# Optimization experiments

Hardware: AMD Instinct MI355X
Metric: run time of the kernel (lower is better)

Reference implementation:

```python
import jax, jax.numpy as jnp
import numpy as np

D = 2            # stalk dimension d
FD = 3           # final_d = d + 1 (add_lp=True, add_hp=False)
HID = 32         # hidden_channels
N_NODES = 50000
E0 = 200000      # undirected edges; directed edge list has 2*E0 entries (second half reversed)
IN_CH = 128
OUT_CH = 32
N_LAYERS = 2
PSIZE = D * (D + 1) // 2  # cayley param size per edge


def _spectral_normalize(W, iters=20):
    # torch spectral_norm: power iteration with detached u, v; sigma = u^T W v
    u = jnp.full((W.shape[0],), 1.0 / np.sqrt(W.shape[0]), W.dtype)
    def body(_, u):
        v = W.T @ u
        v = v / (jnp.linalg.norm(v) + 1e-12)
        u2 = W @ v
        return u2 / (jnp.linalg.norm(u2) + 1e-12)
    u = jax.lax.fori_loop(0, iters, body, u)
    u = jax.lax.stop_gradient(u)
    v = jax.lax.stop_gradient(W.T @ u)
    v = v / (jnp.linalg.norm(v) + 1e-12)
    return W / (u @ W @ v)


def _cayley(p):
    # p: [E, PSIZE] lower-tri params -> skew A -> orthogonal Q = (I - A)^{-1}(I + A)
    E = p.shape[0]
    r, c = jnp.tril_indices(D)
    M = jnp.zeros((E, D, D), p.dtype).at[:, r, c].set(p)
    A = M - jnp.swapaxes(M, 1, 2)
    I = jnp.eye(D, dtype=p.dtype)
    return jnp.linalg.solve(I[None] - A, I[None] + A)


def setup_inputs() -> dict:
    key = jax.random.key(0)
    ks = jax.random.split(key, 8)
    src = jax.random.randint(ks[0], (E0,), 0, N_NODES)
    dst = jax.random.randint(ks[1], (E0,), 0, N_NODES)
    # symmetric directed edge list; edge j and edge j+E0 are reverses of each other
    edge_index = jnp.concatenate([jnp.stack([src, dst]), jnp.stack([dst, src])], axis=1)
    x = jax.random.normal(ks[2], (N_NODES, IN_CH), jnp.float32)
    s = 0.02
    W1 = jax.random.normal(ks[3], (FD * HID, IN_CH), jnp.float32) * s
    b1 = jnp.zeros((FD * HID,), jnp.float32)
    W2 = jax.random.normal(ks[4], (OUT_CH, FD * HID), jnp.float32) * s
    b2 = jnp.zeros((OUT_CH,), jnp.float32)
    W_left = jnp.tile(jnp.eye(FD, dtype=jnp.float32)[None], (N_LAYERS, 1, 1))  # init eye per torch
    W_right = jax.random.normal(ks[5], (N_LAYERS, HID, HID), jnp.float32) / np.sqrt(HID)
    eps = jnp.zeros((N_LAYERS, FD, 1), jnp.float32)
    W_sheaf = jax.random.normal(ks[6], (N_LAYERS, PSIZE, 2 * FD * HID), jnp.float32) * s
    W_wt = jax.random.normal(ks[7], (N_LAYERS, 1, 2 * FD * HID), jnp.float32) * s
    return {"x": x, "edge_index": edge_index, "W1": W1, "b1": b1, "W2": W2, "b2": b2,
            "W_left": W_left, "W_right": W_right, "eps": eps, "W_sheaf": W_sheaf, "W_wt": W_wt}


def reference(x, edge_index, W1, b1, W2, b2, W_left, W_right, eps, W_sheaf, W_wt):
    N = x.shape[0]
    row, col = edge_index[0], edge_index[1]
    e0 = row.shape[0] // 2
    rev = jnp.concatenate([jnp.arange(e0) + e0, jnp.arange(e0)])  # reverse-edge index
    # lin1 + ELU (dropouts = 0 in eval)
    h = jax.nn.elu(x @ W1.T + b1)                 # [N, FD*HID]
    xc = h.reshape(N * FD, HID)                   # [N*FD, HID]
    x0 = xc
    for layer in range(N_LAYERS):
        # --- sheaf learner + edge weight learner (gather endpoint features) ---
        xn = xc.reshape(N, FD * HID)
        cat = jnp.concatenate([xn[row], xn[col]], axis=-1)   # [2*E0, 2*FD*HID]
        p = jnp.tanh(cat @ W_sheaf[layer].T)                 # sheaf map params [2*E0, PSIZE]
        wdir = jax.nn.sigmoid(cat @ W_wt[layer].T)[:, 0]
        w = wdir * wdir[rev]                                 # symmetric edge weight
        # --- normalized connection (bundle) Laplacian ---
        Q = _cayley(p)                                       # per-edge orthogonal maps
        T = jnp.einsum('eij,eik->ejk', Q, Q[rev])            # transport F_u^T F_v
        w2 = w * w
        deg = jax.ops.segment_sum(w2, row, num_segments=N)
        dinv = jnp.where(deg > 0, jax.lax.rsqrt(jnp.maximum(deg, 1e-30)), 0.0)
        cnorm = w2 * dinv[row] * dinv[col]                   # [2*E0]
        # --- left / right weights (spectral-normalized) ---
        Wl = _spectral_normalize(W_left[layer])
        Wr = _spectral_normalize(W_right[layer])
        y = xc.reshape(N, FD, HID)
        y = jnp.einsum('ef,nfh->neh', Wl, y)                 # mix stalk dims
        y = jnp.einsum('neh,ch->nec', y, Wr)                 # mix channels
        # --- apply block-sparse Laplacian: Lx[u] = x[u] - sum_e c_e B_e x[v] ---
        yv = y[col]                                          # gather  [2*E0, FD, HID]
        tv = jnp.concatenate([jnp.einsum('eij,ejh->eih', T, yv[:, :D]), yv[:, D:]], axis=1)
        agg = jax.ops.segment_sum(cnorm[:, None, None] * tv, row, num_segments=N)
        diag = jnp.where(deg > 0, 1.0, 0.0)[:, None, None]
        z = jax.nn.elu((diag * y - agg).reshape(N * FD, HID))
        # --- epsilon-gated residual ---
        coeff = jnp.tile(1.0 + jnp.tanh(eps[layer]), (N, 1))  # [N*FD, 1]
        x0 = coeff * x0 - z
        xc = x0
    return xc.reshape(N, FD * HID) @ W2.T + b2
```

## Files before the change

kernel.cpp:

```cpp
#include <hip/hip_runtime.h>

#define NN 50000
#define E0 200000
#define E2 400000
#define NGROUPS ((NN + 7) / 8)
#define NCHUNK  ((NN + 255) / 256)
#define NTILES  ((NN + 63) / 64)
#define EB      ((E2 + 255) / 256)

typedef __attribute__((ext_vector_type(8))) short short8;
typedef __attribute__((ext_vector_type(4))) float f32x4;

__device__ __forceinline__ float eluf(float x) { return x > 0.0f ? x : expm1f(x); }
__device__ __forceinline__ float fsig(float x) { return 1.0f / (1.0f + __expf(-x)); }
__device__ __forceinline__ float ftanh(float x) {
    float e = __expf(-2.0f * x);
    return (1.0f - e) / (1.0f + e);
}
__device__ __forceinline__ unsigned rne_bf16(float x) {
    unsigned u = __float_as_uint(x);
    return (u + 0x7fffu + ((u >> 16) & 1u)) >> 16;
}

__global__ __launch_bounds__(256) void k_setup(const float* __restrict__ Wl_in, const float* __restrict__ Wr_in,
                                               float* __restrict__ Wl_out, float* __restrict__ Wr_out,
                                               int* __restrict__ cnt, int* __restrict__ fill,
                                               float* __restrict__ deg0, int* __restrict__ gtotal) {
    __shared__ float W[32 * 33];
    __shared__ float us[32], vs[32], tmp[32];
    __shared__ float scal;
    int t = threadIdx.x;
    if (blockIdx.x < 2) {
        int l = blockIdx.x;
        for (int i = t; i < 1024; i += 256) W[(i >> 5) * 33 + (i & 31)] = Wr_in[l * 1024 + i];
        if (t < 32) us[t] = 0.17677669529663688f;
        __syncthreads();
        for (int it = 0; it < 20; ++it) {
            if (t < 32) { float a = 0; for (int r = 0; r < 32; ++r) a = fmaf(W[r * 33 + t], us[r], a); tmp[t] = a; }
            __syncthreads();
            if (t == 0) { float s = 0; for (int c = 0; c < 32; ++c) s += tmp[c] * tmp[c]; scal = 1.0f / (sqrtf(s) + 1e-12f); }
            __syncthreads();
            if (t < 32) vs[t] = tmp[t] * scal;
            __syncthreads();
            if (t < 32) { float a = 0; for (int c = 0; c < 32; ++c) a = fmaf(W[t * 33 + c], vs[c], a); tmp[t] = a; }
            __syncthreads();
            if (t == 0) { float s = 0; for (int r = 0; r < 32; ++r) s += tmp[r] * tmp[r]; scal = 1.0f / (sqrtf(s) + 1e-12f); }
            __syncthreads();
            if (t < 32) us[t] = tmp[t] * scal;
            __syncthreads();
        }
        if (t < 32) { float a = 0; for (int r = 0; r < 32; ++r) a = fmaf(W[r * 33 + t], us[r], a); tmp[t] = a; }
        __syncthreads();
        if (t == 0) {
            float s = 0; for (int c = 0; c < 32; ++c) s += tmp[c] * tmp[c];
            scal = (sqrtf(s) + 1e-12f) / s;
        }
        __syncthreads();
        for (int i = t; i < 1024; i += 256) Wr_out[l * 1024 + i] = W[(i >> 5) * 33 + (i & 31)] * scal;
        if (t == 0) {
            float M[9];
            for (int i = 0; i < 9; ++i) M[i] = Wl_in[l * 9 + i];
            float u[3] = {0.5773502691896258f, 0.5773502691896258f, 0.5773502691896258f};
            float v[3], u2[3];
            for (int it = 0; it < 20; ++it) {
                float s = 0;
                for (int c = 0; c < 3; ++c) { v[c] = M[c] * u[0] + M[3 + c] * u[1] + M[6 + c] * u[2]; s += v[c] * v[c]; }
                float inv = 1.0f / (sqrtf(s) + 1e-12f);
                for (int c = 0; c < 3; ++c) v[c] *= inv;
                s = 0;
                for (int r = 0; r < 3; ++r) { u2[r] = M[r * 3] * v[0] + M[r * 3 + 1] * v[1] + M[r * 3 + 2] * v[2]; s += u2[r] * u2[r]; }
                inv = 1.0f / (sqrtf(s) + 1e-12f);
                for (int r = 0; r < 3; ++r) u[r] = u2[r] * inv;
            }
            float s = 0;
            for (int c = 0; c < 3; ++c) { v[c] = M[c] * u[0] + M[3 + c] * u[1] + M[6 + c] * u[2]; s += v[c] * v[c]; }
            float inv = (sqrtf(s) + 1e-12f) / s;
            for (int i = 0; i < 9; ++i) Wl_out[l * 9 + i] = M[i] * inv;
        }
    } else {
        int base = (blockIdx.x - 2) * 256 + t;
        int stride = (gridDim.x - 2) * 256;
        if (blockIdx.x == 2 && t == 0) *gtotal = 0;
        for (int i = base; i < NN; i += stride) { cnt[i] = 0; fill[i] = 0; deg0[i] = 0.0f; }
    }
}

template<int K, int N, int NH, bool ELU, bool HIST>
__global__ __launch_bounds__(256) void k_gemm(const float* __restrict__ X,
                                              const float* __restrict__ W,
                                              const float* __restrict__ bias,
                                              float* __restrict__ out,
                                              const int* __restrict__ row, int* __restrict__ cnt) {
    constexpr int KP = K + 8;
    constexpr int NT = NH / 16;
    constexpr int KS = K / 32;
    constexpr int NHALVES = N / NH;
    __shared__ __align__(16) unsigned short whi[NH * KP];
    __shared__ __align__(16) unsigned short wlo[NH * KP];
    int tid = threadIdx.x;
    if (HIST) {
        for (int e = blockIdx.x * 256 + tid; e < E2; e += gridDim.x * 256)
            atomicAdd(&cnt[row[e]], 1);
    }
    const int ch = blockIdx.x % NHALVES;
    const int tstream = blockIdx.x / NHALVES;
    const int nstreams = gridDim.x / NHALVES;
    for (int i = tid; i < NH * K; i += 256) {
        float v = W[ch * NH * K + i];
        int r = i / K, c = i % K;
        unsigned h = rne_bf16(v);
        whi[r * KP + c] = (unsigned short)h;
        wlo[r * KP + c] = (unsigned short)rne_bf16(v - __uint_as_float(h << 16));
    }
    __syncthreads();
    int wave = tid >> 6, lane = tid & 63;
    int quad = lane >> 4, r16 = lane & 15;
    for (int t = tstream; t < NTILES; t += nstreams) {
        long m = (long)t * 64 + wave * 16 + r16;
        long mc = m < NN ? m : (NN - 1);
        const float* xrow = X + mc * K + quad * 8;
        short8 ah[KS], al[KS];
#pragma unroll
        for (int ks = 0; ks < KS; ++ks) {
            const float4* xp = (const float4*)(xrow + ks * 32);
            float4 p0 = xp[0], p1 = xp[1];
            float xv[8] = {p0.x, p0.y, p0.z, p0.w, p1.x, p1.y, p1.z, p1.w};
#pragma unroll
            for (int j = 0; j < 8; ++j) {
                unsigned h = rne_bf16(xv[j]);
                ah[ks][j] = (short)h;
                al[ks][j] = (short)rne_bf16(xv[j] - __uint_as_float(h << 16));
            }
        }
        long mbase = (long)t * 64 + wave * 16 + quad * 4;
#pragma unroll
        for (int tt = 0; tt < NT; ++tt) {
            f32x4 acc = (f32x4){0.f, 0.f, 0.f, 0.f};
#pragma unroll
            for (int ks = 0; ks < KS; ++ks) {
                int ro = (tt * 16 + r16) * KP + ks * 32 + quad * 8;
                short8 bh = *(const short8*)&whi[ro];
                short8 bl = *(const short8*)&wlo[ro];
                acc = __builtin_amdgcn_mfma_f32_16x16x32_bf16(ah[ks], bh, acc, 0, 0, 0);
                acc = __builtin_amdgcn_mfma_f32_16x16x32_bf16(al[ks], bh, acc, 0, 0, 0);
                acc = __builtin_amdgcn_mfma_f32_16x16x32_bf16(ah[ks], bl, acc, 0, 0, 0);
            }
            int coln = ch * NH + tt * 16 + r16;
            float b = bias[coln];
#pragma unroll
            for (int rr = 0; rr < 4; ++rr) {
                long mm = mbase + rr;
                if (mm < NN) {
                    float v = acc[rr] + b;
                    if (ELU) v = eluf(v);
                    out[mm * N + coln] = v;
                }
            }
        }
    }
}

__global__ __launch_bounds__(256) void k_scan(const int* __restrict__ cnt, int* __restrict__ start,
                                              int* __restrict__ gtotal) {
    __shared__ int s[256];
    __shared__ int soff;
    int b = blockIdx.x, t = threadIdx.x;
    int i = b * 256 + t;
    int v = (i < NN) ? cnt[i] : 0;
    s[t] = v;
    __syncthreads();
    for (int off = 1; off < 256; off <<= 1) {
        int add = (t >= off) ? s[t - off] : 0;
        __syncthreads();
        s[t] += add;
        __syncthreads();
    }
    if (t == 255) soff = atomicAdd(gtotal, s[255]);
    __syncthreads();
    if (i < NN) start[i] = s[t] - v + soff;
}

__global__ __launch_bounds__(256) void k_filly8(const float* __restrict__ xc,
                                                const float* __restrict__ Wl, const float* __restrict__ Wr,
                                                const float* __restrict__ Wsh, const float* __restrict__ Wwt,
                                                unsigned* __restrict__ yA, unsigned short* __restrict__ yB,
                                                float4* __restrict__ proj,
                                                const int* __restrict__ row, const int* __restrict__ start,
                                                int* __restrict__ fill, int* __restrict__ eslot) {
    int tid = threadIdx.x;
    if (blockIdx.x >= NGROUPS) {
        int e = (blockIdx.x - NGROUPS) * 256 + tid;
        if (e < E2) {
            int u = row[e];
            eslot[e] = start[u] + atomicAdd(&fill[u], 1);
        }
        return;
    }
    __shared__ float wrs[32 * 33];
    __shared__ float wls[9];
    __shared__ float xcs[8][96];
    __shared__ float ws1[192], wt[192];
    int n0 = blockIdx.x * 8;
    for (int i = tid; i < 1024; i += 256) wrs[(i >> 5) * 33 + (i & 31)] = Wr[i];
    if (tid < 9) wls[tid] = Wl[tid];
    if (tid < 192) {
        ws1[tid] = Wsh[192 + tid];
        wt[tid]  = Wwt[tid];
    }
    for (int i = tid; i < 192; i += 256) {
        int nd = i / 24, of = (i % 24) * 4;
        *(float4*)&xcs[nd][of] = *(const float4*)&xc[(n0 + nd) * 96 + of];
    }
    __syncthreads();
    int node = tid >> 5, c = tid & 31;
    int n = n0 + node;
    float a1 = 0, a2 = 0, a3 = 0, a4 = 0;
#pragma unroll
    for (int j = 0; j < 3; ++j) {
        int k = j * 32 + c;
        float xv = xcs[node][k];
        a1 = fmaf(xv, ws1[k], a1);
        a2 = fmaf(xv, ws1[96 + k], a2);
        a3 = fmaf(xv, wt[k], a3);
        a4 = fmaf(xv, wt[96 + k], a4);
    }
#pragma unroll
    for (int off = 16; off; off >>= 1) {
        a1 += __shfl_xor(a1, off);
        a2 += __shfl_xor(a2, off);
        a3 += __shfl_xor(a3, off);
        a4 += __shfl_xor(a4, off);
    }
    if (c == 0) proj[n] = make_float4(a1, a2, a3, a4);
    {
        float t0 = 0, t1 = 0, t2 = 0;
        const float* wr = &wrs[c * 33];
        const float* xr = xcs[node];
#pragma unroll
        for (int h = 0; h < 32; ++h) {
            float w = wr[h];
            t0 = fmaf(xr[h], w, t0);
            t1 = fmaf(xr[32 + h], w, t1);
            t2 = fmaf(xr[64 + h], w, t2);
        }
        float o0 = wls[0] * t0 + wls[1] * t1 + wls[2] * t2;
        float o1 = wls[3] * t0 + wls[4] * t1 + wls[5] * t2;
        float o2 = wls[6] * t0 + wls[7] * t1 + wls[8] * t2;
        yA[n * 32 + c] = rne_bf16(o0) | (rne_bf16(o1) << 16);
        yB[n * 32 + c] = (unsigned short)rne_bf16(o2);
    }
}

__global__ __launch_bounds__(256) void k_coef(const int* __restrict__ row, const int* __restrict__ col,
                                              const int* __restrict__ eslot,
                                              const float4* __restrict__ proj,
                                              uint2* __restrict__ meta, float* __restrict__ deg) {
    int e = blockIdx.x * 256 + threadIdx.x;
    if (e >= E0) return;
    int u = row[e], v = col[e];
    float4 pu = proj[u], pv = proj[v];
    float a_e = ftanh(pu.x + pv.y);
    float a_r = ftanh(pv.x + pu.y);
    float wd_e = fsig(pu.z + pv.w);
    float wd_r = fsig(pv.z + pu.w);
    float w = wd_e * wd_r;
    float w2 = w * w;
    float ie = 1.0f / (1.0f + a_e * a_e), ir = 1.0f / (1.0f + a_r * a_r);
    float ce = (1.0f - a_e * a_e) * ie, se = 2.0f * a_e * ie;
    float cr = (1.0f - a_r * a_r) * ir, sr = 2.0f * a_r * ir;
    float C = ce * cr + se * sr;
    float S = ce * sr - se * cr;
    unsigned cb = rne_bf16(C), sb = rne_bf16(S), wb = rne_bf16(w2);
    meta[eslot[e]]      = make_uint2(cb | (sb << 16), (unsigned)v | (wb << 16));
    meta[eslot[e + E0]] = make_uint2(cb | ((sb ^ 0x8000u) << 16), (unsigned)u | (wb << 16));
    atomicAdd(&deg[u], w2);
    atomicAdd(&deg[v], w2);
}

__device__ __forceinline__ void gather_accum(int s0, int ec, int c,
                                             const uint2* __restrict__ meta,
                                             const float* __restrict__ deg, float du,
                                             const unsigned* __restrict__ yA,
                                             const unsigned short* __restrict__ yB,
                                             float& acc0, float& acc1, float& acc2) {
    for (int bs = 0; bs < ec; bs += 32) {
        int nb2 = min(32, ec - bs);
        float CC = 0, SS = 0, cnl = 0;
        int vj = 0;
        if (c < nb2) {
            uint2 mt = meta[s0 + bs + c];
            vj = (int)(mt.y & 0xffffu);
            float w2 = __uint_as_float(mt.y & 0xffff0000u);
            float Cv = __uint_as_float(mt.x << 16);
            float Sv = __uint_as_float(mt.x & 0xffff0000u);
            float dv = deg[vj];
            float dvi = dv > 0.0f ? rsqrtf(fmaxf(dv, 1e-30f)) : 0.0f;
            cnl = w2 * du * dvi;
            CC = cnl * Cv;
            SS = cnl * Sv;
        }
        int j4 = nb2 & ~3;
        int j = 0;
        for (; j < j4; j += 4) {
#pragma unroll
            for (int jj = 0; jj < 4; ++jj) {
                float Cj = __shfl(CC, j + jj, 32);
                float Sj = __shfl(SS, j + jj, 32);
                float cj = __shfl(cnl, j + jj, 32);
                int v = __shfl(vj, j + jj, 32);
                unsigned ua = yA[v * 32 + c];
                unsigned ub = (unsigned)yB[v * 32 + c];
                float y0 = __uint_as_float(ua << 16);
                float y1 = __uint_as_float(ua & 0xffff0000u);
                float y2 = __uint_as_float(ub << 16);
                acc0 = fmaf(Cj, y0, acc0);
                acc0 = fmaf(-Sj, y1, acc0);
                acc1 = fmaf(Sj, y0, acc1);
                acc1 = fmaf(Cj, y1, acc1);
                acc2 = fmaf(cj, y2, acc2);
            }
        }
        for (; j < nb2; ++j) {
            float Cj = __shfl(CC, j, 32);
            float Sj = __shfl(SS, j, 32);
            float cj = __shfl(cnl, j, 32);
            int v = __shfl(vj, j, 32);
            unsigned ua = yA[v * 32 + c];
            unsigned ub = (unsigned)yB[v * 32 + c];
            float y0 = __uint_as_float(ua << 16);
            float y1 = __uint_as_float(ua & 0xffff0000u);
            float y2 = __uint_as_float(ub << 16);
            acc0 = fmaf(Cj, y0, acc0);
            acc0 = fmaf(-Sj, y1, acc0);
            acc1 = fmaf(Sj, y0, acc1);
            acc1 = fmaf(Cj, y1, acc1);
            acc2 = fmaf(cj, y2, acc2);
        }
    }
}

__global__ __launch_bounds__(256) void k_gatherY(const int* __restrict__ start,
                                                 const int* __restrict__ cnt,
                                                 const uint2* __restrict__ meta,
                                                 const float* __restrict__ deg0,
                                                 const unsigned* __restrict__ yA0,
                                                 const unsigned short* __restrict__ yB0,
                                                 const float* __restrict__ eps,
                                                 float* __restrict__ xc,
                                                 const float* __restrict__ Wl, const float* __restrict__ Wr,
                                                 const float* __restrict__ Wsh, const float* __restrict__ Wwt,
                                                 unsigned* __restrict__ yA1, unsigned short* __restrict__ yB1,
                                                 float4* __restrict__ proj, float* __restrict__ deg1) {
    __shared__ float wrs[32 * 33];
    __shared__ float wls[9];
    __shared__ float xcs[8][96];
    __shared__ float ws1[192], wt[192];
    int tid = threadIdx.x;
    for (int i = tid; i < 1024; i += 256) wrs[(i >> 5) * 33 + (i & 31)] = Wr[i];
    if (tid < 9) wls[tid] = Wl[tid];
    if (tid < 192) {
        ws1[tid] = Wsh[(1 * 3 + 1) * 192 + tid];
        wt[tid]  = Wwt[1 * 192 + tid];
    }
    int node = tid >> 5, c = tid & 31;
    int n = blockIdx.x * 8 + node;
    int s0 = start[n], ec = cnt[n];
    float dn = deg0[n];
    float du = dn > 0.0f ? rsqrtf(fmaxf(dn, 1e-30f)) : 0.0f;
    float acc0 = 0, acc1 = 0, acc2 = 0;
    gather_accum(s0, ec, c, meta, deg0, du, yA0, yB0, acc0, acc1, acc2);
    float diag = dn > 0.0f ? 1.0f : 0.0f;
    unsigned ua = yA0[n * 32 + c];
    unsigned ub = (unsigned)yB0[n * 32 + c];
    float oy0 = __uint_as_float(ua << 16);
    float oy1 = __uint_as_float(ua & 0xffff0000u);
    float oy2 = __uint_as_float(ub << 16);
    float c0 = 1.0f + tanhf(eps[0]);
    float c1 = 1.0f + tanhf(eps[1]);
    float c2 = 1.0f + tanhf(eps[2]);
    int base = n * 96 + c;
    float nx0 = c0 * xc[base]      - eluf(diag * oy0 - acc0);
    float nx1 = c1 * xc[base + 32] - eluf(diag * oy1 - acc1);
    float nx2 = c2 * xc[base + 64] - eluf(diag * oy2 - acc2);
    xc[base] = nx0; xc[base + 32] = nx1; xc[base + 64] = nx2;
    if (c == 0) deg1[n] = 0.0f;
    xcs[node][c] = nx0; xcs[node][32 + c] = nx1; xcs[node][64 + c] = nx2;
    __syncthreads();
    float a1 = nx0 * ws1[c] + nx1 * ws1[32 + c] + nx2 * ws1[64 + c];
    float a2 = nx0 * ws1[96 + c] + nx1 * ws1[128 + c] + nx2 * ws1[160 + c];
    float a3 = nx0 * wt[c] + nx1 * wt[32 + c] + nx2 * wt[64 + c];
    float a4 = nx0 * wt[96 + c] + nx1 * wt[128 + c] + nx2 * wt[160 + c];
#pragma unroll
    for (int off = 16; off; off >>= 1) {
        a1 += __shfl_xor(a1, off);
        a2 += __shfl_xor(a2, off);
        a3 += __shfl_xor(a3, off);
        a4 += __shfl_xor(a4, off);
    }
    if (c == 0) proj[n] = make_float4(a1, a2, a3, a4);
    {
        float t0 = 0, t1 = 0, t2 = 0;
        const float* wr = &wrs[c * 33];
        const float* xr = xcs[node];
#pragma unroll
        for (int h = 0; h < 32; ++h) {
            float w = wr[h];
            t0 = fmaf(xr[h], w, t0);
            t1 = fmaf(xr[32 + h], w, t1);
            t2 = fmaf(xr[64 + h], w, t2);
        }
        float o0 = wls[0] * t0 + wls[1] * t1 + wls[2] * t2;
        float o1 = wls[3] * t0 + wls[4] * t1 + wls[5] * t2;
        float o2 = wls[6] * t0 + wls[7] * t1 + wls[8] * t2;
        yA1[n * 32 + c] = rne_bf16(o0) | (rne_bf16(o1) << 16);
        yB1[n * 32 + c] = (unsigned short)rne_bf16(o2);
    }
}

__global__ __launch_bounds__(256) void k_gather(const int* __restrict__ start,
                                                const int* __restrict__ cnt,
                                                const uint2* __restrict__ meta,
                                                const float* __restrict__ deg,
                                                const unsigned* __restrict__ yA,
                                                const unsigned short* __restrict__ yB,
                                                const float* __restrict__ eps,
                                                int layer, float* __restrict__ xc) {
    int tid = threadIdx.x;
    int node = tid >> 5, c = tid & 31;
    int n = blockIdx.x * 8 + node;
    if (n >= NN) return;
    int s0 = start[n], ec = cnt[n];
    float dn = deg[n];
    float du = dn > 0.0f ? rsqrtf(fmaxf(dn, 1e-30f)) : 0.0f;
    float acc0 = 0, acc1 = 0, acc2 = 0;
    gather_accum(s0, ec, c, meta, deg, du, yA, yB, acc0, acc1, acc2);
    float diag = dn > 0.0f ? 1.0f : 0.0f;
    unsigned ua = yA[n * 32 + c];
    unsigned ub = (unsigned)yB[n * 32 + c];
    float oy0 = __uint_as_float(ua << 16);
    float oy1 = __uint_as_float(ua & 0xffff0000u);
    float oy2 = __uint_as_float(ub << 16);
    float c0 = 1.0f + tanhf(eps[layer * 3 + 0]);
    float c1 = 1.0f + tanhf(eps[layer * 3 + 1]);
    float c2 = 1.0f + tanhf(eps[layer * 3 + 2]);
    int base = n * 96 + c;
    float z0 = eluf(diag * oy0 - acc0);
    float z1 = eluf(diag * oy1 - acc1);
    float z2 = eluf(diag * oy2 - acc2);
    xc[base]      = c0 * xc[base]      - z0;
    xc[base + 32] = c1 * xc[base + 32] - z1;
    xc[base + 64] = c2 * xc[base + 64] - z2;
}

extern "C" void kernel_launch(void* const* d_in, const int* in_sizes, int n_in,
                              void* d_out, int out_size, void* d_ws, size_t ws_size,
                              hipStream_t stream) {
    const float* x     = (const float*)d_in[0];
    const int*   ei    = (const int*)d_in[1];
    const float* W1    = (const float*)d_in[2];
    const float* b1    = (const float*)d_in[3];
    const float* W2    = (const float*)d_in[4];
    const float* b2    = (const float*)d_in[5];
    const float* Wl    = (const float*)d_in[6];
    const float* Wr    = (const float*)d_in[7];
    const float* eps   = (const float*)d_in[8];
    const float* Wsh   = (const float*)d_in[9];
    const float* Wwt   = (const float*)d_in[10];
    float* out = (float*)d_out;
    const int* row = ei;
    const int* col = ei + E2;

    char* pc = (char*)d_ws;
    float* xc     = (float*)pc;          pc += (size_t)NN * 96 * 4;
    uint2* meta   = (uint2*)pc;          pc += (size_t)E2 * 8;
    unsigned* yA0 = (unsigned*)pc;       pc += (size_t)NN * 32 * 4;
    unsigned* yA1 = (unsigned*)pc;       pc += (size_t)NN * 32 * 4;
    unsigned short* yB0 = (unsigned short*)pc; pc += (size_t)NN * 32 * 2;
    unsigned short* yB1 = (unsigned short*)pc; pc += (size_t)NN * 32 * 2;
    pc = (char*)(((size_t)pc + 15) & ~(size_t)15);
    float4* proj  = (float4*)pc;         pc += (size_t)NN * 16;
    float* deg0   = (float*)pc;          pc += (size_t)NN * 4;
    float* deg1   = (float*)pc;          pc += (size_t)NN * 4;
    float* Wl_n   = (float*)pc;          pc += 32 * 4;
    float* Wr_n   = (float*)pc;          pc += 2048 * 4;
    int* cnt      = (int*)pc;            pc += (size_t)NN * 4;
    int* start    = (int*)pc;            pc += (size_t)NN * 4;
    int* fill     = (int*)pc;            pc += (size_t)NN * 4;
    int* eslot    = (int*)pc;            pc += (size_t)E2 * 4;
    int* gtotal   = (int*)pc;            pc += 4;

    k_setup<<<34, 256, 0, stream>>>(Wl, Wr, Wl_n, Wr_n, cnt, fill, deg0, gtotal);
    k_gemm<128, 96, 48, true, true><<<512, 256, 0, stream>>>(x, W1, b1, xc, row, cnt);
    k_scan<<<NCHUNK, 256, 0, stream>>>(cnt, start, gtotal);
    k_filly8<<<NGROUPS + EB, 256, 0, stream>>>(xc, Wl_n, Wr_n, Wsh, Wwt,
                                               yA0, yB0, proj, row, start, fill, eslot);
    k_coef<<<(E0 + 255) / 256, 256, 0, stream>>>(row, col, eslot, proj, meta, deg0);
    k_gatherY<<<NGROUPS, 256, 0, stream>>>(start, cnt, meta, deg0, yA0, yB0, eps, xc,
                                           Wl_n + 9, Wr_n + 1024, Wsh, Wwt, yA1, yB1, proj, deg1);
    k_coef<<<(E0 + 255) / 256, 256, 0, stream>>>(row, col, eslot, proj, meta, deg1);
    k_gather<<<NGROUPS, 256, 0, stream>>>(start, cnt, meta, deg1, yA1, yB1, eps, 1, xc);
    k_gemm<96, 32, 32, false, false><<<512, 256, 0, stream>>>(xc, W2, b2, out, nullptr, nullptr);
}
```

Measured before the change: 321.7 us.

## Split gather across two half-waves per node, pack y into uint2, move spectral norm into gemm

```diff
diff --git a/kernel.cpp b/kernel.cpp
--- a/kernel.cpp
+++ b/kernel.cpp
@@ -4,6 +4,7 @@
 #define E0 200000
 #define E2 400000
 #define NGROUPS ((NN + 7) / 8)
+#define NG4     ((NN + 3) / 4)
 #define NCHUNK  ((NN + 255) / 256)
 #define NTILES  ((NN + 63) / 64)
 #define EB      ((E2 + 255) / 256)
@@ -22,89 +23,96 @@
     return (u + 0x7fffu + ((u >> 16) & 1u)) >> 16;
 }
 
-__global__ __launch_bounds__(256) void k_setup(const float* __restrict__ Wl_in, const float* __restrict__ Wr_in,
-                                               float* __restrict__ Wl_out, float* __restrict__ Wr_out,
-                                               int* __restrict__ cnt, int* __restrict__ fill,
+__global__ __launch_bounds__(256) void k_setup(int* __restrict__ cnt, int* __restrict__ fill,
                                                float* __restrict__ deg0, int* __restrict__ gtotal) {
+    int i = blockIdx.x * 256 + threadIdx.x;
+    if (i == 0) *gtotal = 0;
+    if (i < NN) { cnt[i] = 0; fill[i] = 0; deg0[i] = 0.0f; }
+}
+
+__device__ __forceinline__ void spectral_block(int l, const float* __restrict__ Wl_in,
+                                               const float* __restrict__ Wr_in,
+                                               float* __restrict__ Wl_out, float* __restrict__ Wr_out) {
     __shared__ float W[32 * 33];
     __shared__ float us[32], vs[32], tmp[32];
     __shared__ float scal;
     int t = threadIdx.x;
-    if (blockIdx.x < 2) {
-        int l = blockIdx.x;
-        for (int i = t; i < 1024; i += 256) W[(i >> 5) * 33 + (i & 31)] = Wr_in[l * 1024 + i];
-        if (t < 32) us[t] = 0.17677669529663688f;
-        __syncthreads();
+    for (int i = t; i < 1024; i += 256) W[(i >> 5) * 33 + (i & 31)] = Wr_in[l * 1024 + i];
+    if (t < 32) us[t] = 0.17677669529663688f;
+    __syncthreads();
+    for (int it = 0; it < 20; ++it) {
+        if (t < 32) { float a = 0; for (int r = 0; r < 32; ++r) a = fmaf(W[r * 33 + t], us[r], a); tmp[t] = a; }
+        __syncthreads();
+        if (t == 0) { float s = 0; for (int c = 0; c < 32; ++c) s += tmp[c] * tmp[c]; scal = 1.0f / (sqrtf(s) + 1e-12f); }
+        __syncthreads();
+        if (t < 32) vs[t] = tmp[t] * scal;
+        __syncthreads();
+        if (t < 32) { float a = 0; for (int c = 0; c < 32; ++c) a = fmaf(W[t * 33 + c], vs[c], a); tmp[t] = a; }
+        __syncthreads();
+        if (t == 0) { float s = 0; for (int r = 0; r < 32; ++r) s += tmp[r] * tmp[r]; scal = 1.0f / (sqrtf(s) + 1e-12f); }
+        __syncthreads();
+        if (t < 32) us[t] = tmp[t] * scal;
+        __syncthreads();
+    }
+    if (t < 32) { float a = 0; for (int r = 0; r < 32; ++r) a = fmaf(W[r * 33 + t], us[r], a); tmp[t] = a; }
+    __syncthreads();
+    if (t == 0) {
+        float s = 0; for (int c = 0; c < 32; ++c) s += tmp[c] * tmp[c];
+        scal = (sqrtf(s) + 1e-12f) / s;
+    }
+    __syncthreads();
+    for (int i = t; i < 1024; i += 256) Wr_out[l * 1024 + i] = W[(i >> 5) * 33 + (i & 31)] * scal;
+    if (t == 0) {
+        float M[9];
+        for (int i = 0; i < 9; ++i) M[i] = Wl_in[l * 9 + i];
+        float u[3] = {0.5773502691896258f, 0.5773502691896258f, 0.5773502691896258f};
+        float v[3], u2[3];
         for (int it = 0; it < 20; ++it) {
-            if (t < 32) { float a = 0; for (int r = 0; r < 32; ++r) a = fmaf(W[r * 33 + t], us[r], a); tmp[t] = a; }
-            __syncthreads();
-            if (t == 0) { float s = 0; for (int c = 0; c < 32; ++c) s += tmp[c] * tmp[c]; scal = 1.0f / (sqrtf(s) + 1e-12f); }
-            __syncthreads();
-            if (t < 32) vs[t] = tmp[t] * scal;
-            __syncthreads();
-            if (t < 32) { float a = 0; for (int c = 0; c < 32; ++c) a = fmaf(W[t * 33 + c], vs[c], a); tmp[t] = a; }
-            __syncthreads();
-            if (t == 0) { float s = 0; for (int r = 0; r < 32; ++r) s += tmp[r] * tmp[r]; scal = 1.0f / (sqrtf(s) + 1e-12f); }
-            __syncthreads();
-            if (t < 32) us[t] = tmp[t] * scal;
-            __syncthreads();
-        }
-        if (t < 32) { float a = 0; for (int r = 0; r < 32; ++r) a = fmaf(W[r * 33 + t], us[r], a); tmp[t] = a; }
-        __syncthreads();
-        if (t == 0) {
-            float s = 0; for (int c = 0; c < 32; ++c) s += tmp[c] * tmp[c];
-            scal = (sqrtf(s) + 1e-12f) / s;
-        }
-        __syncthreads();
-        for (int i = t; i < 1024; i += 256) Wr_out[l * 1024 + i] = W[(i >> 5) * 33 + (i & 31)] * scal;
-        if (t == 0) {
-            float M[9];
-            for (int i = 0; i < 9; ++i) M[i] = Wl_in[l * 9 + i];
-            float u[3] = {0.5773502691896258f, 0.5773502691896258f, 0.5773502691896258f};
-            float v[3], u2[3];
-            for (int it = 0; it < 20; ++it) {
-                float s = 0;
-                for (int c = 0; c < 3; ++c) { v[c] = M[c] * u[0] + M[3 + c] * u[1] + M[6 + c] * u[2]; s += v[c] * v[c]; }
-                float inv = 1.0f / (sqrtf(s) + 1e-12f);
-                for (int c = 0; c < 3; ++c) v[c] *= inv;
-                s = 0;
-                for (int r = 0; r < 3; ++r) { u2[r] = M[r * 3] * v[0] + M[r * 3 + 1] * v[1] + M[r * 3 + 2] * v[2]; s += u2[r] * u2[r]; }
-                inv = 1.0f / (sqrtf(s) + 1e-12f);
-                for (int r = 0; r < 3; ++r) u[r] = u2[r] * inv;
-            }
             float s = 0;
             for (int c = 0; c < 3; ++c) { v[c] = M[c] * u[0] + M[3 + c] * u[1] + M[6 + c] * u[2]; s += v[c] * v[c]; }
-            float inv = (sqrtf(s) + 1e-12f) / s;
-            for (int i = 0; i < 9; ++i) Wl_out[l * 9 + i] = M[i] * inv;
-        }
-    } else {
-        int base = (blockIdx.x - 2) * 256 + t;
-        int stride = (gridDim.x - 2) * 256;
-        if (blockIdx.x == 2 && t == 0) *gtotal = 0;
-        for (int i = base; i < NN; i += stride) { cnt[i] = 0; fill[i] = 0; deg0[i] = 0.0f; }
-    }
-}
-
-template<int K, int N, int NH, bool ELU, bool HIST>
+            float inv = 1.0f / (sqrtf(s) + 1e-12f);
+            for (int c = 0; c < 3; ++c) v[c] *= inv;
+            s = 0;
+            for (int r = 0; r < 3; ++r) { u2[r] = M[r * 3] * v[0] + M[r * 3 + 1] * v[1] + M[r * 3 + 2] * v[2]; s += u2[r] * u2[r]; }
+            inv = 1.0f / (sqrtf(s) + 1e-12f);
+            for (int r = 0; r < 3; ++r) u[r] = u2[r] * inv;
+        }
+        float s = 0;
+        for (int c = 0; c < 3; ++c) { v[c] = M[c] * u[0] + M[3 + c] * u[1] + M[6 + c] * u[2]; s += v[c] * v[c]; }
+        float inv = (sqrtf(s) + 1e-12f) / s;
+        for (int i = 0; i < 9; ++i) Wl_out[l * 9 + i] = M[i] * inv;
+    }
+}
+
+template<int K, int N, int NH, bool ELU, bool AUX>
 __global__ __launch_bounds__(256) void k_gemm(const float* __restrict__ X,
                                               const float* __restrict__ W,
                                               const float* __restrict__ bias,
                                               float* __restrict__ out,
-                                              const int* __restrict__ row, int* __restrict__ cnt) {
+                                              const int* __restrict__ row, int* __restrict__ cnt,
+                                              const float* __restrict__ Wl_in, const float* __restrict__ Wr_in,
+                                              float* __restrict__ Wl_out, float* __restrict__ Wr_out) {
     constexpr int KP = K + 8;
     constexpr int NT = NH / 16;
     constexpr int KS = K / 32;
     constexpr int NHALVES = N / NH;
+    const int nmain = AUX ? (int)gridDim.x - 2 : (int)gridDim.x;
+    if constexpr (AUX) {
+        if ((int)blockIdx.x >= nmain) {
+            spectral_block((int)blockIdx.x - nmain, Wl_in, Wr_in, Wl_out, Wr_out);
+            return;
+        }
+    }
     __shared__ __align__(16) unsigned short whi[NH * KP];
     __shared__ __align__(16) unsigned short wlo[NH * KP];
     int tid = threadIdx.x;
-    if (HIST) {
-        for (int e = blockIdx.x * 256 + tid; e < E2; e += gridDim.x * 256)
+    if constexpr (AUX) {
+        for (int e = blockIdx.x * 256 + tid; e < E2; e += nmain * 256)
             atomicAdd(&cnt[row[e]], 1);
     }
     const int ch = blockIdx.x % NHALVES;
     const int tstream = blockIdx.x / NHALVES;
-    const int nstreams = gridDim.x / NHALVES;
+    const int nstreams = nmain / NHALVES;
     for (int i = tid; i < NH * K; i += 256) {
         float v = W[ch * NH * K + i];
         int r = i / K, c = i % K;
@@ -183,7 +191,7 @@
 __global__ __launch_bounds__(256) void k_filly8(const float* __restrict__ xc,
                                                 const float* __restrict__ Wl, const float* __restrict__ Wr,
                                                 const float* __restrict__ Wsh, const float* __restrict__ Wwt,
-                                                unsigned* __restrict__ yA, unsigned short* __restrict__ yB,
+                                                uint2* __restrict__ yAB,
                                                 float4* __restrict__ proj,
                                                 const int* __restrict__ row, const int* __restrict__ start,
                                                 int* __restrict__ fill, int* __restrict__ eslot) {
@@ -246,8 +254,7 @@
         float o0 = wls[0] * t0 + wls[1] * t1 + wls[2] * t2;
         float o1 = wls[3] * t0 + wls[4] * t1 + wls[5] * t2;
         float o2 = wls[6] * t0 + wls[7] * t1 + wls[8] * t2;
-        yA[n * 32 + c] = rne_bf16(o0) | (rne_bf16(o1) << 16);
-        yB[n * 32 + c] = (unsigned short)rne_bf16(o2);
+        yAB[n * 32 + c] = make_uint2(rne_bf16(o0) | (rne_bf16(o1) << 16), rne_bf16(o2) << 16);
     }
 }
 
@@ -277,18 +284,19 @@
     atomicAdd(&deg[v], w2);
 }
 
-__device__ __forceinline__ void gather_accum(int s0, int ec, int c,
+__device__ __forceinline__ void gather_accum(int s0, int ec, int h, int c,
                                              const uint2* __restrict__ meta,
                                              const float* __restrict__ deg, float du,
-                                             const unsigned* __restrict__ yA,
-                                             const unsigned short* __restrict__ yB,
+                                             const uint2* __restrict__ yAB,
                                              float& acc0, float& acc1, float& acc2) {
-    for (int bs = 0; bs < ec; bs += 32) {
-        int nb2 = min(32, ec - bs);
+    const uint2* yc = yAB + c;
+    for (int bs = 0; bs < ec; bs += 64) {
+        int nb = min(64, ec - bs);
         float CC = 0, SS = 0, cnl = 0;
         int vj = 0;
-        if (c < nb2) {
-            uint2 mt = meta[s0 + bs + c];
+        int eidx = 2 * c + h;
+        if (eidx < nb) {
+            uint2 mt = meta[s0 + bs + eidx];
             vj = (int)(mt.y & 0xffffu);
             float w2 = __uint_as_float(mt.y & 0xffff0000u);
             float Cv = __uint_as_float(mt.x << 16);
@@ -299,7 +307,8 @@
             CC = cnl * Cv;
             SS = cnl * Sv;
         }
-        int j4 = nb2 & ~3;
+        int jmax = (nb + 1 - h) >> 1;
+        int j4 = jmax & ~3;
         int j = 0;
         for (; j < j4; j += 4) {
 #pragma unroll
@@ -308,11 +317,10 @@
                 float Sj = __shfl(SS, j + jj, 32);
                 float cj = __shfl(cnl, j + jj, 32);
                 int v = __shfl(vj, j + jj, 32);
-                unsigned ua = yA[v * 32 + c];
-                unsigned ub = (unsigned)yB[v * 32 + c];
-                float y0 = __uint_as_float(ua << 16);
-                float y1 = __uint_as_float(ua & 0xffff0000u);
-                float y2 = __uint_as_float(ub << 16);
+                uint2 y = yc[v * 32];
+                float y0 = __uint_as_float(y.x << 16);
+                float y1 = __uint_as_float(y.x & 0xffff0000u);
+                float y2 = __uint_as_float(y.y);
                 acc0 = fmaf(Cj, y0, acc0);
                 acc0 = fmaf(-Sj, y1, acc0);
                 acc1 = fmaf(Sj, y0, acc1);
@@ -320,16 +328,15 @@
                 acc2 = fmaf(cj, y2, acc2);
             }
         }
-        for (; j < nb2; ++j) {
+        for (; j < jmax; ++j) {
             float Cj = __shfl(CC, j, 32);
             float Sj = __shfl(SS, j, 32);
             float cj = __shfl(cnl, j, 32);
             int v = __shfl(vj, j, 32);
-            unsigned ua = yA[v * 32 + c];
-            unsigned ub = (unsigned)yB[v * 32 + c];
-            float y0 = __uint_as_float(ua << 16);
-            float y1 = __uint_as_float(ua & 0xffff0000u);
-            float y2 = __uint_as_float(ub << 16);
+            uint2 y = yc[v * 32];
+            float y0 = __uint_as_float(y.x << 16);
+            float y1 = __uint_as_float(y.x & 0xffff0000u);
+            float y2 = __uint_as_float(y.y);
             acc0 = fmaf(Cj, y0, acc0);
             acc0 = fmaf(-Sj, y1, acc0);
             acc1 = fmaf(Sj, y0, acc1);
@@ -343,49 +350,53 @@
                                                  const int* __restrict__ cnt,
                                                  const uint2* __restrict__ meta,
                                                  const float* __restrict__ deg0,
-                                                 const unsigned* __restrict__ yA0,
-                                                 const unsigned short* __restrict__ yB0,
+                                                 const uint2* __restrict__ yAB0,
                                                  const float* __restrict__ eps,
                                                  float* __restrict__ xc,
                                                  const float* __restrict__ Wl, const float* __restrict__ Wr,
                                                  const float* __restrict__ Wsh, const float* __restrict__ Wwt,
-                                                 unsigned* __restrict__ yA1, unsigned short* __restrict__ yB1,
+                                                 uint2* __restrict__ yAB1,
                                                  float4* __restrict__ proj, float* __restrict__ deg1) {
     __shared__ float wrs[32 * 33];
     __shared__ float wls[9];
-    __shared__ float xcs[8][96];
+    __shared__ float xcs[4][96];
     __shared__ float ws1[192], wt[192];
     int tid = threadIdx.x;
     for (int i = tid; i < 1024; i += 256) wrs[(i >> 5) * 33 + (i & 31)] = Wr[i];
     if (tid < 9) wls[tid] = Wl[tid];
     if (tid < 192) {
         ws1[tid] = Wsh[(1 * 3 + 1) * 192 + tid];
-        wt[tid]  = Wwt[1 * 192 + tid];
-    }
-    int node = tid >> 5, c = tid & 31;
-    int n = blockIdx.x * 8 + node;
+        wt[tid]  = Wwt[192 + tid];
+    }
+    int wv = tid >> 6, lane = tid & 63, h = lane >> 5, c = lane & 31;
+    int n = blockIdx.x * 4 + wv;
     int s0 = start[n], ec = cnt[n];
     float dn = deg0[n];
     float du = dn > 0.0f ? rsqrtf(fmaxf(dn, 1e-30f)) : 0.0f;
-    float acc0 = 0, acc1 = 0, acc2 = 0;
-    gather_accum(s0, ec, c, meta, deg0, du, yA0, yB0, acc0, acc1, acc2);
-    float diag = dn > 0.0f ? 1.0f : 0.0f;
-    unsigned ua = yA0[n * 32 + c];
-    unsigned ub = (unsigned)yB0[n * 32 + c];
-    float oy0 = __uint_as_float(ua << 16);
-    float oy1 = __uint_as_float(ua & 0xffff0000u);
-    float oy2 = __uint_as_float(ub << 16);
+    int base = n * 96 + c;
+    float xv0 = xc[base], xv1 = xc[base + 32], xv2 = xc[base + 64];
+    uint2 yown = yAB0[n * 32 + c];
     float c0 = 1.0f + tanhf(eps[0]);
     float c1 = 1.0f + tanhf(eps[1]);
     float c2 = 1.0f + tanhf(eps[2]);
-    int base = n * 96 + c;
-    float nx0 = c0 * xc[base]      - eluf(diag * oy0 - acc0);
-    float nx1 = c1 * xc[base + 32] - eluf(diag * oy1 - acc1);
-    float nx2 = c2 * xc[base + 64] - eluf(diag * oy2 - acc2);
-    xc[base] = nx0; xc[base + 32] = nx1; xc[base + 64] = nx2;
-    if (c == 0) deg1[n] = 0.0f;
-    xcs[node][c] = nx0; xcs[node][32 + c] = nx1; xcs[node][64 + c] = nx2;
-    __syncthreads();
+    __syncthreads();
+    float acc0 = 0, acc1 = 0, acc2 = 0;
+    gather_accum(s0, ec, h, c, meta, deg0, du, yAB0, acc0, acc1, acc2);
+    acc0 += __shfl_xor(acc0, 32);
+    acc1 += __shfl_xor(acc1, 32);
+    acc2 += __shfl_xor(acc2, 32);
+    float diag = dn > 0.0f ? 1.0f : 0.0f;
+    float oy0 = __uint_as_float(yown.x << 16);
+    float oy1 = __uint_as_float(yown.x & 0xffff0000u);
+    float oy2 = __uint_as_float(yown.y);
+    float nx0 = c0 * xv0 - eluf(diag * oy0 - acc0);
+    float nx1 = c1 * xv1 - eluf(diag * oy1 - acc1);
+    float nx2 = c2 * xv2 - eluf(diag * oy2 - acc2);
+    if (h == 0) {
+        xc[base] = nx0; xc[base + 32] = nx1; xc[base + 64] = nx2;
+        xcs[wv][c] = nx0; xcs[wv][32 + c] = nx1; xcs[wv][64 + c] = nx2;
+        if (c == 0) deg1[n] = 0.0f;
+    }
     float a1 = nx0 * ws1[c] + nx1 * ws1[32 + c] + nx2 * ws1[64 + c];
     float a2 = nx0 * ws1[96 + c] + nx1 * ws1[128 + c] + nx2 * ws1[160 + c];
     float a3 = nx0 * wt[c] + nx1 * wt[32 + c] + nx2 * wt[64 + c];
@@ -397,23 +408,26 @@
         a3 += __shfl_xor(a3, off);
         a4 += __shfl_xor(a4, off);
     }
-    if (c == 0) proj[n] = make_float4(a1, a2, a3, a4);
-    {
-        float t0 = 0, t1 = 0, t2 = 0;
-        const float* wr = &wrs[c * 33];
-        const float* xr = xcs[node];
-#pragma unroll
-        for (int h = 0; h < 32; ++h) {
-            float w = wr[h];
-            t0 = fmaf(xr[h], w, t0);
-            t1 = fmaf(xr[32 + h], w, t1);
-            t2 = fmaf(xr[64 + h], w, t2);
-        }
+    if (lane == 0) proj[n] = make_float4(a1, a2, a3, a4);
+    __syncthreads();
+    float t0 = 0, t1 = 0, t2 = 0;
+    const float* wr = &wrs[c * 33 + h * 16];
+    const float* xr = &xcs[wv][h * 16];
+#pragma unroll
+    for (int k = 0; k < 16; ++k) {
+        float w = wr[k];
+        t0 = fmaf(xr[k], w, t0);
+        t1 = fmaf(xr[32 + k], w, t1);
+        t2 = fmaf(xr[64 + k], w, t2);
+    }
+    t0 += __shfl_xor(t0, 32);
+    t1 += __shfl_xor(t1, 32);
+    t2 += __shfl_xor(t2, 32);
+    if (h == 0) {
         float o0 = wls[0] * t0 + wls[1] * t1 + wls[2] * t2;
         float o1 = wls[3] * t0 + wls[4] * t1 + wls[5] * t2;
         float o2 = wls[6] * t0 + wls[7] * t1 + wls[8] * t2;
-        yA1[n * 32 + c] = rne_bf16(o0) | (rne_bf16(o1) << 16);
-        yB1[n * 32 + c] = (unsigned short)rne_bf16(o2);
+        yAB1[n * 32 + c] = make_uint2(rne_bf16(o0) | (rne_bf16(o1) << 16), rne_bf16(o2) << 16);
     }
 }
 
@@ -421,35 +435,35 @@
                                                 const int* __restrict__ cnt,
                                                 const uint2* __restrict__ meta,
                                                 const float* __restrict__ deg,
-                                                const unsigned* __restrict__ yA,
-                                                const unsigned short* __restrict__ yB,
+                                                const uint2* __restrict__ yAB,
                                                 const float* __restrict__ eps,
                                                 int layer, float* __restrict__ xc) {
     int tid = threadIdx.x;
-    int node = tid >> 5, c = tid & 31;
-    int n = blockIdx.x * 8 + node;
-    if (n >= NN) return;
+    int lane = tid & 63, h = lane >> 5, c = lane & 31;
+    int n = blockIdx.x * 4 + (tid >> 6);
     int s0 = start[n], ec = cnt[n];
     float dn = deg[n];
     float du = dn > 0.0f ? rsqrtf(fmaxf(dn, 1e-30f)) : 0.0f;
-    float acc0 = 0, acc1 = 0, acc2 = 0;
-    gather_accum(s0, ec, c, meta, deg, du, yA, yB, acc0, acc1, acc2);
-    float diag = dn > 0.0f ? 1.0f : 0.0f;
-    unsigned ua = yA[n * 32 + c];
-    unsigned ub = (unsigned)yB[n * 32 + c];
-    float oy0 = __uint_as_float(ua << 16);
-    float oy1 = __uint_as_float(ua & 0xffff0000u);
-    float oy2 = __uint_as_float(ub << 16);
+    int base = n * 96 + c;
+    float xv0 = xc[base], xv1 = xc[base + 32], xv2 = xc[base + 64];
+    uint2 yown = yAB[n * 32 + c];
     float c0 = 1.0f + tanhf(eps[layer * 3 + 0]);
     float c1 = 1.0f + tanhf(eps[layer * 3 + 1]);
     float c2 = 1.0f + tanhf(eps[layer * 3 + 2]);
-    int base = n * 96 + c;
-    float z0 = eluf(diag * oy0 - acc0);
-    float z1 = eluf(diag * oy1 - acc1);
-    float z2 = eluf(diag * oy2 - acc2);
-    xc[base]      = c0 * xc[base]      - z0;
-    xc[base + 32] = c1 * xc[base + 32] - z1;
-    xc[base + 64] = c2 * xc[base + 64] - z2;
+    float acc0 = 0, acc1 = 0, acc2 = 0;
+    gather_accum(s0, ec, h, c, meta, deg, du, yAB, acc0, acc1, acc2);
+    acc0 += __shfl_xor(acc0, 32);
+    acc1 += __shfl_xor(acc1, 32);
+    acc2 += __shfl_xor(acc2, 32);
+    if (h == 0) {
+        float diag = dn > 0.0f ? 1.0f : 0.0f;
+        float oy0 = __uint_as_float(yown.x << 16);
+        float oy1 = __uint_as_float(yown.x & 0xffff0000u);
+        float oy2 = __uint_as_float(yown.y);
+        xc[base]      = c0 * xv0 - eluf(diag * oy0 - acc0);
+        xc[base + 32] = c1 * xv1 - eluf(diag * oy1 - acc1);
+        xc[base + 64] = c2 * xv2 - eluf(diag * oy2 - acc2);
+    }
 }
 
 extern "C" void kernel_launch(void* const* d_in, const int* in_sizes, int n_in,
@@ -473,10 +487,8 @@
     char* pc = (char*)d_ws;
     float* xc     = (float*)pc;          pc += (size_t)NN * 96 * 4;
     uint2* meta   = (uint2*)pc;          pc += (size_t)E2 * 8;
-    unsigned* yA0 = (unsigned*)pc;       pc += (size_t)NN * 32 * 4;
-    unsigned* yA1 = (unsigned*)pc;       pc += (size_t)NN * 32 * 4;
-    unsigned short* yB0 = (unsigned short*)pc; pc += (size_t)NN * 32 * 2;
-    unsigned short* yB1 = (unsigned short*)pc; pc += (size_t)NN * 32 * 2;
+    uint2* yAB0   = (uint2*)pc;          pc += (size_t)NN * 32 * 8;
+    uint2* yAB1   = (uint2*)pc;          pc += (size_t)NN * 32 * 8;
     pc = (char*)(((size_t)pc + 15) & ~(size_t)15);
     float4* proj  = (float4*)pc;         pc += (size_t)NN * 16;
     float* deg0   = (float*)pc;          pc += (size_t)NN * 4;
@@ -489,15 +501,17 @@
     int* eslot    = (int*)pc;            pc += (size_t)E2 * 4;
     int* gtotal   = (int*)pc;            pc += 4;
 
-    k_setup<<<34, 256, 0, stream>>>(Wl, Wr, Wl_n, Wr_n, cnt, fill, deg0, gtotal);
-    k_gemm<128, 96, 48, true, true><<<512, 256, 0, stream>>>(x, W1, b1, xc, row, cnt);
+    k_setup<<<NCHUNK, 256, 0, stream>>>(cnt, fill, deg0, gtotal);
+    k_gemm<128, 96, 48, true, true><<<514, 256, 0, stream>>>(x, W1, b1, xc, row, cnt,
+                                                             Wl, Wr, Wl_n, Wr_n);
     k_scan<<<NCHUNK, 256, 0, stream>>>(cnt, start, gtotal);
     k_filly8<<<NGROUPS + EB, 256, 0, stream>>>(xc, Wl_n, Wr_n, Wsh, Wwt,
-                                               yA0, yB0, proj, row, start, fill, eslot);
+                                               yAB0, proj, row, start, fill, eslot);
     k_coef<<<(E0 + 255) / 256, 256, 0, stream>>>(row, col, eslot, proj, meta, deg0);
-    k_gatherY<<<NGROUPS, 256, 0, stream>>>(start, cnt, meta, deg0, yA0, yB0, eps, xc,
-                                           Wl_n + 9, Wr_n + 1024, Wsh, Wwt, yA1, yB1, proj, deg1);
+    k_gatherY<<<NG4, 256, 0, stream>>>(start, cnt, meta, deg0, yAB0, eps, xc,
+                                       Wl_n + 9, Wr_n + 1024, Wsh, Wwt, yAB1, proj, deg1);
     k_coef<<<(E0 + 255) / 256, 256, 0, stream>>>(row, col, eslot, proj, meta, deg1);
-    k_gather<<<NGROUPS, 256, 0, stream>>>(start, cnt, meta, deg1, yA1, yB1, eps, 1, xc);
-    k_gemm<96, 32, 32, false, false><<<512, 256, 0, stream>>>(xc, W2, b2, out, nullptr, nullptr);
-}
+    k_gather<<<NG4, 256, 0, stream>>>(start, cnt, meta, deg1, yAB1, eps, 1, xc);
+    k_gemm<96, 32, 32, false, false><<<512, 256, 0, stream>>>(xc, W2, b2, out, nullptr, nullptr,
+                                                              nullptr, nullptr, nullptr, nullptr);
+}
```

After: 327.9 us. About the same (+1.9%).
